# Performance work log

Measured on AMD Instinct MI355X. Metric: run time of the kernel, lower is better.

The kernel has to match this reference:

```python
import jax, jax.numpy as jnp
import numpy as np

B, C, H, W = 16, 512, 32, 32
NH = 8
HD = C // NH


def setup_inputs() -> dict:
    key = jax.random.key(0)
    k1, k2, k3 = jax.random.split(key, 3)
    x = jax.random.normal(k1, (B, C, H, W), dtype=jnp.float32)
    w_qkv = jax.random.normal(k2, (3 * C, C), dtype=jnp.float32) * (1.0 / np.sqrt(C))
    w_proj = jax.random.normal(k3, (C, C), dtype=jnp.float32) * (1.0 / np.sqrt(C))
    b_proj = jnp.zeros((C,), dtype=jnp.float32)
    return {"x": x, "w_qkv": w_qkv, "w_proj": w_proj, "b_proj": b_proj}


def reference(x, w_qkv, w_proj, b_proj):
    b, c, h, w = x.shape
    n = h * w
    # 1x1 conv qkv: (3C, C) applied per pixel
    qkv = jnp.einsum('oc,bchw->bohw', w_qkv, x)  # [B, 3C, H, W]
    qkv = qkv.reshape(b, 3, NH, HD, n)           # [B, 3, nh, hd, N]
    qkv = jnp.transpose(qkv, (1, 0, 2, 4, 3))    # [3, B, nh, N, hd]
    q, k, v = qkv[0], qkv[1], qkv[2]
    scale = HD ** -0.5
    scores = jnp.einsum('bhnd,bhmd->bhnm', q, k) * scale  # [B, nh, N, N]
    attn = jax.nn.softmax(scores, axis=-1)
    out = jnp.einsum('bhnm,bhmd->bhnd', attn, v)          # [B, nh, N, hd]
    out = jnp.transpose(out, (0, 1, 3, 2)).reshape(b, c, h, w)
    # 1x1 conv proj with bias
    out = jnp.einsum('oc,bchw->bohw', w_proj, out) + b_proj[None, :, None, None]
    return out
```

## Files before the change

### kernel.cpp

```cpp
#include <hip/hip_runtime.h>
#include <hip/hip_bf16.h>
#include <math.h>

#define BB 16
#define CC 512
#define NH 8
#define HD 64
#define NN 1024
#define THREEC 1536

#define QSCALE 0.18033688f

typedef __attribute__((ext_vector_type(8))) short bf16x8;
typedef __attribute__((ext_vector_type(4))) float f32x4;
typedef __attribute__((ext_vector_type(16))) float f32x16;

#if __has_builtin(__builtin_amdgcn_exp2f)
#define EXP2F __builtin_amdgcn_exp2f
#else
#define EXP2F exp2f
#endif

#define XT_OFF 0u
#define WQ_OFF 16777216u
#define WP_OFF 18350080u
#define QB_OFF 18874368u
#define KB_OFF 35651584u
#define VT_OFF 52428800u
#define AB_OFF 69206016u

static __device__ inline unsigned short f2bf(float f) {
  union { float f; unsigned u; } v; v.f = f;
  unsigned r = v.u + 0x7fffu + ((v.u >> 16) & 1u);
  return (unsigned short)(r >> 16);
}

static __device__ inline unsigned pk2bf(float a, float b) {
#if defined(__AMDGCN__) && __has_builtin(__builtin_amdgcn_cvt_pk_bf16_f32)
  typedef __attribute__((ext_vector_type(2))) __bf16 bfp2;
  union { bfp2 v; unsigned u; } z;
  z.v = __builtin_amdgcn_cvt_pk_bf16_f32(a, b);
  return z.u;
#else
  return (unsigned)f2bf(a) | ((unsigned)f2bf(b) << 16);
#endif
}

static __device__ inline void gld_lds16(const unsigned short* g, unsigned short* l) {
  __builtin_amdgcn_global_load_lds(
      (const __attribute__((address_space(1))) unsigned int*)g,
      (__attribute__((address_space(3))) unsigned int*)l, 16, 0, 0);
}

__global__ __launch_bounds__(256) void prep_w(const float* __restrict__ wqkv,
                                              const float* __restrict__ wproj,
                                              unsigned short* __restrict__ dq,
                                              unsigned short* __restrict__ dp) {
  const size_t i8 = ((size_t)blockIdx.x * 256 + threadIdx.x) * 8;
  const float* src;
  unsigned short* dst;
  if (i8 < 786432u) { src = wqkv + i8; dst = dq + i8; }
  else              { src = wproj + (i8 - 786432u); dst = dp + (i8 - 786432u); }
  float4 a = *(const float4*)src;
  float4 b = *(const float4*)(src + 4);
  unsigned short pk[8] = {f2bf(a.x), f2bf(a.y), f2bf(a.z), f2bf(a.w),
                          f2bf(b.x), f2bf(b.y), f2bf(b.z), f2bf(b.w)};
  *(uint4*)dst = *(const uint4*)pk;
}

__global__ __launch_bounds__(256) void prep_xT(const float* __restrict__ x,
                                               unsigned short* __restrict__ xT) {
  const int b  = blockIdx.z;
  const int c0 = blockIdx.y * 64;
  const int n0 = blockIdx.x * 64;
  __shared__ float tile[64][65];
  const int t  = threadIdx.x;
  const int cl = t >> 4, n4 = (t & 15) * 4;
#pragma unroll
  for (int r = 0; r < 4; ++r) {
    float4 v = *(const float4*)&x[((size_t)b * CC + c0 + cl + 16 * r) * NN + n0 + n4];
    *(float4*)&tile[cl + 16 * r][n4] = v;
  }
  __syncthreads();
  const int nl = t >> 4, c4 = (t & 15) * 4;
#pragma unroll
  for (int r = 0; r < 4; ++r) {
    ushort4 p;
    p.x = f2bf(tile[c4 + 0][nl + 16 * r]);
    p.y = f2bf(tile[c4 + 1][nl + 16 * r]);
    p.z = f2bf(tile[c4 + 2][nl + 16 * r]);
    p.w = f2bf(tile[c4 + 3][nl + 16 * r]);
    *(ushort4*)&xT[((size_t)b * NN + n0 + nl + 16 * r) * CC + c0 + c4] = p;
  }
}

__global__ __launch_bounds__(256) void qkv_mfma(const unsigned short* __restrict__ wq,
                                                const unsigned short* __restrict__ xT,
                                                unsigned short* __restrict__ qb,
                                                unsigned short* __restrict__ kb_,
                                                unsigned short* __restrict__ vt) {
  const int b  = blockIdx.z;
  const int o0 = blockIdx.y * 128;
  const int n0 = blockIdx.x * 128;
  const int t  = threadIdx.x;
  const int w    = t >> 6;
  const int lane = t & 63;
  const int quad = lane >> 4;
  const int l16  = lane & 15;
  const int m_off = (w >> 1) * 64;
  const int n_off = (w & 1) * 64;

  __shared__ unsigned short sm[17408];
  unsigned short* As = sm;
  unsigned short* Bs = sm + 8192;

  const int which = o0 >> 9;
  const bool vmode = (which == 2);

  const int srow = lane >> 3;
  const int ssw  = ((lane & 7) ^ srow) * 8;
  const unsigned short* gA = wq + (size_t)(o0 + 32 * w + srow) * CC + ssw;
  const unsigned short* gB = xT + ((size_t)b * NN + n0 + 32 * w + srow) * CC + ssw;

  f32x4 acc[4][4] = {};

  for (int c0 = 0; c0 < CC; c0 += 64) {
    __syncthreads();
#pragma unroll
    for (int L = 0; L < 4; ++L) {
      gld_lds16(gA + (size_t)(8 * L) * CC + c0, &As[(32 * w + 8 * L) * 64]);
      gld_lds16(gB + (size_t)(8 * L) * CC + c0, &Bs[(32 * w + 8 * L) * 64]);
    }
    __syncthreads();
    const unsigned short* Af = vmode ? Bs : As;
    const unsigned short* Bf = vmode ? As : Bs;
#pragma unroll
    for (int ks = 0; ks < 2; ++ks) {
      const int ph = ((ks * 4 + quad) ^ (l16 & 7)) * 8;
      bf16x8 af[4], bfr[4];
#pragma unroll
      for (int i = 0; i < 4; ++i) {
        af[i]  = *(const bf16x8*)&Af[(m_off + 16 * i + l16) * 64 + ph];
        bfr[i] = *(const bf16x8*)&Bf[(n_off + 16 * i + l16) * 64 + ph];
      }
#pragma unroll
      for (int i = 0; i < 4; ++i)
#pragma unroll
        for (int j = 0; j < 4; ++j)
          acc[i][j] = __builtin_amdgcn_mfma_f32_16x16x32_bf16(af[i], bfr[j], acc[i][j], 0, 0, 0);
    }
  }

  __syncthreads();
  const float sc = (which == 0) ? QSCALE : 1.0f;
#pragma unroll
  for (int i = 0; i < 4; ++i) {
#pragma unroll
    for (int j = 0; j < 4; ++j) {
      const int Drow = m_off + 16 * i + quad * 4;
      const int Dcol = n_off + 16 * j + l16;
      ushort4 p;
      p.x = f2bf(acc[i][j][0] * sc);
      p.y = f2bf(acc[i][j][1] * sc);
      p.z = f2bf(acc[i][j][2] * sc);
      p.w = f2bf(acc[i][j][3] * sc);
      *(ushort4*)&sm[Dcol * 136 + Drow] = p;
    }
  }
  __syncthreads();
  const int lrow = t >> 1;
  const int half = t & 1;
  const unsigned short* src = &sm[lrow * 136 + 64 * half];
  if (!vmode) {
    const int hh = ((o0 >> 6) & 7) + half;
    unsigned short* dst = (which == 0 ? qb : kb_) +
        ((size_t)(b * NH + hh) * NN + n0 + lrow) * HD;
#pragma unroll
    for (int i = 0; i < 8; ++i) *(uint4*)(dst + 8 * i) = *(const uint4*)(src + 8 * i);
  } else {
    const int hh = ((o0 + lrow) >> 6) & 7;
    const int d  = lrow & 63;
    unsigned short* dst = vt + ((size_t)(b * NH + hh) * HD + d) * NN + n0 + 64 * half;
#pragma unroll
    for (int i = 0; i < 8; ++i) *(uint4*)(dst + 8 * i) = *(const uint4*)(src + 8 * i);
  }
}

__global__ __launch_bounds__(128) void attn_mfma(const unsigned short* __restrict__ Qg,
                                                 const unsigned short* __restrict__ Kg,
                                                 const unsigned short* __restrict__ Vtg,
                                                 unsigned short* __restrict__ attnB) {
  const int bh = blockIdx.x;
  const int b  = bh >> 3;
  const int h  = bh & 7;
  const int n0 = blockIdx.y * 128;
  const int t  = threadIdx.x;
  const int w    = t >> 6;
  const int lane = t & 63;
  const int l31  = lane & 31;
  const int hi   = lane >> 5;

  __shared__ unsigned short sm[9216];
  unsigned short* Ks = sm;
  unsigned short* Vt = sm + 4608;

  const unsigned short* qbase = Qg + ((size_t)bh * NN + n0 + 64 * w) * HD + hi * 8;
  bf16x8 qf[2][4];
#pragma unroll
  for (int qs = 0; qs < 2; ++qs)
#pragma unroll
    for (int c = 0; c < 4; ++c)
      qf[qs][c] = *(const bf16x8*)(qbase + (size_t)(32 * qs + l31) * HD + 16 * c);

  const int krow = (l31 & ~12) | ((l31 & 4) << 1) | ((l31 & 8) >> 1);
  const int fk   = ((krow >> 3) & 1) * 4;
  const int fv   = ((l31 >> 3) & 1) * 4;

  f32x16 oacc[2][2] = {};
  float lacc[2] = {0.f, 0.f};

  int sOff[9];
#pragma unroll
  for (int s = 0; s < 9; ++s) {
    const int idx = 64 * s + lane;
    const int row = (idx * 7282) >> 16;
    const int scol = idx - 9 * row;
    const int fR  = ((row >> 3) & 1) * 4;
    const int g   = (scol < 8) ? (scol ^ fR) : 0;
    sOff[s] = (w == 0) ? (row * HD + g * 8) : (row * NN + g * 8);
  }
  const unsigned short* gsrc = (w == 0)
      ? (Kg + (size_t)bh * NN * HD)
      : (Vtg + (size_t)bh * HD * NN);
  const int tstep = (w == 0) ? 64 * HD : 64;
  unsigned short* sdst = (w == 0) ? Ks : Vt;

#pragma unroll 1
  for (int j0 = 0; j0 < NN; j0 += 64) {
    __syncthreads();
#pragma unroll
    for (int s = 0; s < 9; ++s) gld_lds16(gsrc + sOff[s], sdst + 512 * s);
    gsrc += tstep;
    __syncthreads();

#pragma unroll
    for (int kb = 0; kb < 2; ++kb) {
      bf16x8 kf[4];
      const unsigned short* krp = Ks + (32 * kb + krow) * 72;
#pragma unroll
      for (int c = 0; c < 4; ++c)
        kf[c] = *(const bf16x8*)(krp + ((2 * c + hi) ^ fk) * 8);
      bf16x8 vf[2][2];
#pragma unroll
      for (int mt = 0; mt < 2; ++mt) {
        const unsigned short* vrp = Vt + (32 * mt + l31) * 72;
#pragma unroll
        for (int g = 0; g < 2; ++g)
          vf[g][mt] = *(const bf16x8*)(vrp + ((4 * kb + 2 * g + hi) ^ fv) * 8);
      }
#pragma unroll
      for (int qs = 0; qs < 2; ++qs) {
        f32x16 st = {};
#pragma unroll
        for (int c = 0; c < 4; ++c)
          st = __builtin_amdgcn_mfma_f32_32x32x16_bf16(kf[c], qf[qs][c], st, 0, 0, 0);
        float e[16];
#pragma unroll
        for (int r = 0; r < 16; ++r) { e[r] = EXP2F(st[r]); lacc[qs] += e[r]; }
        unsigned P[8];
#pragma unroll
        for (int i = 0; i < 8; ++i) P[i] = pk2bf(e[2 * i], e[2 * i + 1]);
#pragma unroll
        for (int g = 0; g < 2; ++g) {
          union { unsigned u[4]; bf16x8 v; } cv;
          cv.u[0] = P[4 * g + 0]; cv.u[1] = P[4 * g + 1];
          cv.u[2] = P[4 * g + 2]; cv.u[3] = P[4 * g + 3];
#pragma unroll
          for (int mt = 0; mt < 2; ++mt)
            oacc[qs][mt] = __builtin_amdgcn_mfma_f32_32x32x16_bf16(
                vf[g][mt], cv.v, oacc[qs][mt], 0, 0, 0);
        }
      }
    }
  }

  float inv[2];
#pragma unroll
  for (int qs = 0; qs < 2; ++qs) {
    float l = lacc[qs];
    l += __shfl_xor(l, 32);
    inv[qs] = 1.0f / l;
  }

  __syncthreads();
  unsigned short* Es = sm + w * 4608;
#pragma unroll
  for (int qs = 0; qs < 2; ++qs) {
#pragma unroll
    for (int mt = 0; mt < 2; ++mt) {
#pragma unroll
      for (int rr = 0; rr < 4; ++rr) {
        const int d = 32 * mt + 8 * rr + 4 * hi;
        ushort4 p;
        p.x = f2bf(oacc[qs][mt][4 * rr + 0] * inv[qs]);
        p.y = f2bf(oacc[qs][mt][4 * rr + 1] * inv[qs]);
        p.z = f2bf(oacc[qs][mt][4 * rr + 2] * inv[qs]);
        p.w = f2bf(oacc[qs][mt][4 * rr + 3] * inv[qs]);
        *(ushort4*)&Es[(32 * qs + l31) * 72 + d] = p;
      }
    }
  }
  const int half = lane & 1;
#pragma unroll
  for (int p = 0; p < 2; ++p) {
    const int q = 32 * p + (lane >> 1);
    const unsigned short* src = &Es[q * 72 + 32 * half];
    unsigned short* gdst = attnB + ((size_t)b * NN + n0 + 64 * w + q) * CC +
                           h * HD + 32 * half;
#pragma unroll
    for (int i = 0; i < 4; ++i) *(uint4*)(gdst + 8 * i) = *(const uint4*)(src + 8 * i);
  }
}

__global__ __launch_bounds__(256) void proj_mfma(const unsigned short* __restrict__ wp,
                                                 const unsigned short* __restrict__ aB,
                                                 const float* __restrict__ bias,
                                                 float* __restrict__ out) {
  const int b  = blockIdx.z;
  const int o0 = blockIdx.y * 128;
  const int n0 = blockIdx.x * 128;
  const int t  = threadIdx.x;
  const int w    = t >> 6;
  const int lane = t & 63;
  const int quad = lane >> 4;
  const int l16  = lane & 15;
  const int m_off = (w >> 1) * 64;
  const int n_off = (w & 1) * 64;

  __shared__ unsigned short sm[16384];
  unsigned short* As = sm;
  unsigned short* Bs = sm + 8192;

  const int srow = lane >> 3;
  const int ssw  = ((lane & 7) ^ srow) * 8;
  const unsigned short* gA = wp + (size_t)(o0 + 32 * w + srow) * CC + ssw;
  const unsigned short* gB = aB + ((size_t)b * NN + n0 + 32 * w + srow) * CC + ssw;

  f32x4 acc[4][4] = {};

  for (int c0 = 0; c0 < CC; c0 += 64) {
    __syncthreads();
#pragma unroll
    for (int L = 0; L < 4; ++L) {
      gld_lds16(gA + (size_t)(8 * L) * CC + c0, &As[(32 * w + 8 * L) * 64]);
      gld_lds16(gB + (size_t)(8 * L) * CC + c0, &Bs[(32 * w + 8 * L) * 64]);
    }
    __syncthreads();
#pragma unroll
    for (int ks = 0; ks < 2; ++ks) {
      const int ph = ((ks * 4 + quad) ^ (l16 & 7)) * 8;
      bf16x8 af[4], bfr[4];
#pragma unroll
      for (int i = 0; i < 4; ++i) {
        af[i]  = *(const bf16x8*)&As[(m_off + 16 * i + l16) * 64 + ph];
        bfr[i] = *(const bf16x8*)&Bs[(n_off + 16 * i + l16) * 64 + ph];
      }
#pragma unroll
      for (int i = 0; i < 4; ++i)
#pragma unroll
        for (int j = 0; j < 4; ++j)
          acc[i][j] = __builtin_amdgcn_mfma_f32_16x16x32_bf16(af[i], bfr[j], acc[i][j], 0, 0, 0);
    }
  }

#pragma unroll
  for (int i = 0; i < 4; ++i) {
#pragma unroll
    for (int r = 0; r < 4; ++r) {
      const int o = o0 + m_off + 16 * i + quad * 4 + r;
      const float bv = bias[o];
      float* orow = out + ((size_t)b * CC + o) * NN + n0 + n_off;
#pragma unroll
      for (int j = 0; j < 4; ++j)
        orow[16 * j + l16] = acc[i][j][r] + bv;
    }
  }
}

extern "C" void kernel_launch(void* const* d_in, const int* in_sizes, int n_in,
                              void* d_out, int out_size, void* d_ws, size_t ws_size,
                              hipStream_t stream) {
  const float* x      = (const float*)d_in[0];
  const float* w_qkv  = (const float*)d_in[1];
  const float* w_proj = (const float*)d_in[2];
  const float* b_proj = (const float*)d_in[3];
  char* wsb  = (char*)d_ws;
  float* out = (float*)d_out;

  unsigned short* xT  = (unsigned short*)(wsb + XT_OFF);
  unsigned short* wq  = (unsigned short*)(wsb + WQ_OFF);
  unsigned short* wp  = (unsigned short*)(wsb + WP_OFF);
  unsigned short* qb  = (unsigned short*)(wsb + QB_OFF);
  unsigned short* kb_ = (unsigned short*)(wsb + KB_OFF);
  unsigned short* vt  = (unsigned short*)(wsb + VT_OFF);
  unsigned short* aB  = (unsigned short*)(wsb + AB_OFF);

  prep_w<<<512, 256, 0, stream>>>(w_qkv, w_proj, wq, wp);
  prep_xT<<<dim3(16, 8, BB), 256, 0, stream>>>(x, xT);
  qkv_mfma<<<dim3(8, 12, BB), 256, 0, stream>>>(wq, xT, qb, kb_, vt);
  attn_mfma<<<dim3(BB * NH, NN / 128), 128, 0, stream>>>(qb, kb_, vt, aB);
  proj_mfma<<<dim3(8, 4, BB), 256, 0, stream>>>(wp, aB, b_proj, out);
}
```

Baseline: 213.0 us.

## Double-buffer K/V tiles in attention and widen blocks to four waves

The attention kernel now runs 256 threads (four waves) per block covering 256 query rows, so each block shares one K/V tile load across twice as many queries. The K and V^T tiles are double-buffered in shared memory: the next tile's global-to-LDS loads are issued before computing on the current one, which removes one barrier per iteration and overlaps loads with MFMA work. This doubles the LDS footprint per block and halves the grid size (512 blocks), which may reduce occupancy and how well work spreads across CUs. The load loop relies on the first barrier of the next iteration to also cover arrival of the prefetched tile, so correctness depends on gld_lds16 completing by that barrier.

Measured after the change: 210.5 us. Within noise of the previous version (-1.2%).

```diff
diff --git a/kernel.cpp b/kernel.cpp
--- a/kernel.cpp
+++ b/kernel.cpp
@@ -186,23 +186,21 @@
   }
 }
 
-__global__ __launch_bounds__(128) void attn_mfma(const unsigned short* __restrict__ Qg,
+__global__ __launch_bounds__(256) void attn_mfma(const unsigned short* __restrict__ Qg,
                                                  const unsigned short* __restrict__ Kg,
                                                  const unsigned short* __restrict__ Vtg,
                                                  unsigned short* __restrict__ attnB) {
   const int bh = blockIdx.x;
   const int b  = bh >> 3;
   const int h  = bh & 7;
-  const int n0 = blockIdx.y * 128;
+  const int n0 = blockIdx.y * 256;
   const int t  = threadIdx.x;
   const int w    = t >> 6;
   const int lane = t & 63;
   const int l31  = lane & 31;
   const int hi   = lane >> 5;
 
-  __shared__ unsigned short sm[9216];
-  unsigned short* Ks = sm;
-  unsigned short* Vt = sm + 4608;
+  __shared__ unsigned short sm[18432];
 
   const unsigned short* qbase = Qg + ((size_t)bh * NN + n0 + 64 * w) * HD + hi * 8;
   bf16x8 qf[2][4];
@@ -219,29 +217,38 @@
   f32x16 oacc[2][2] = {};
   float lacc[2] = {0.f, 0.f};
 
-  int sOff[9];
-#pragma unroll
-  for (int s = 0; s < 9; ++s) {
-    const int idx = 64 * s + lane;
+  const bool kv = (w >= 2);
+  int sOff[5];
+#pragma unroll
+  for (int s = 0; s < 5; ++s) {
+    const int idx = 128 * s + (w & 1) * 64 + lane;
     const int row = (idx * 7282) >> 16;
     const int scol = idx - 9 * row;
     const int fR  = ((row >> 3) & 1) * 4;
     const int g   = (scol < 8) ? (scol ^ fR) : 0;
-    sOff[s] = (w == 0) ? (row * HD + g * 8) : (row * NN + g * 8);
-  }
-  const unsigned short* gsrc = (w == 0)
-      ? (Kg + (size_t)bh * NN * HD)
-      : (Vtg + (size_t)bh * HD * NN);
-  const int tstep = (w == 0) ? 64 * HD : 64;
-  unsigned short* sdst = (w == 0) ? Ks : Vt;
+    sOff[s] = kv ? (row * NN + g * 8) : (row * HD + g * 8);
+  }
+  const unsigned short* gbase = kv ? (Vtg + (size_t)bh * HD * NN)
+                                   : (Kg + (size_t)bh * NN * HD);
+  const int gstep = kv ? 64 : 64 * HD;
+  unsigned short* lbase = sm + (kv ? 4608 : 0) + ((w & 1) * 64) * 8;
+
+#pragma unroll
+  for (int s = 0; s < 5; ++s)
+    if (s < 4 || (w & 1) == 0) gld_lds16(gbase + sOff[s], lbase + 1024 * s);
 
 #pragma unroll 1
-  for (int j0 = 0; j0 < NN; j0 += 64) {
+  for (int jt = 0; jt < 16; ++jt) {
     __syncthreads();
-#pragma unroll
-    for (int s = 0; s < 9; ++s) gld_lds16(gsrc + sOff[s], sdst + 512 * s);
-    gsrc += tstep;
-    __syncthreads();
+    if (jt < 15) {
+      const unsigned short* gn = gbase + (size_t)(jt + 1) * gstep;
+      unsigned short* ln = lbase + ((jt + 1) & 1) * 9216;
+#pragma unroll
+      for (int s = 0; s < 5; ++s)
+        if (s < 4 || (w & 1) == 0) gld_lds16(gn + sOff[s], ln + 1024 * s);
+    }
+    const unsigned short* Ks = sm + (jt & 1) * 9216;
+    const unsigned short* Vt = Ks + 4608;
 
 #pragma unroll
     for (int kb = 0; kb < 2; ++kb) {
@@ -408,6 +415,6 @@
   prep_w<<<512, 256, 0, stream>>>(w_qkv, w_proj, wq, wp);
   prep_xT<<<dim3(16, 8, BB), 256, 0, stream>>>(x, xT);
   qkv_mfma<<<dim3(8, 12, BB), 256, 0, stream>>>(wq, xT, qb, kb_, vt);
-  attn_mfma<<<dim3(BB * NH, NN / 128), 128, 0, stream>>>(qb, kb_, vt, aB);
+  attn_mfma<<<dim3(BB * NH, NN / 256), 256, 0, stream>>>(qb, kb_, vt, aB);
   proj_mfma<<<dim3(8, 4, BB), 256, 0, stream>>>(wp, aB, b_proj, out);
 }
```
